# Kernel optimization log

Hardware: AMD Instinct MI355X
Metric: run time of the kernel (lower is better)

The kernel has to match this reference:

```python
import jax, jax.numpy as jnp
import numpy as np

B, C, H, Wd = 256, 2048, 14, 14
E, A = 16, 3000  # num experts (DESC_INDEX), num answers (ANSWER_INDEX)


def setup_inputs() -> dict:
    key = jax.random.key(0)
    k1, k2, k3, k4, k5 = jax.random.split(key, 5)
    return {
        "mask": jax.random.uniform(k1, (B, 1, H, Wd), dtype=jnp.float32),
        "features": jax.random.normal(k2, (B, C, H, Wd), dtype=jnp.float32),
        "W": jax.random.normal(k3, (E, A, C), dtype=jnp.float32) * 0.02,
        "b": jax.random.normal(k4, (E, A), dtype=jnp.float32) * 0.02,
        "inst": jax.random.randint(k5, (B,), 0, E, dtype=jnp.int64),
    }


def reference(mask, features, W, b, inst):
    Bn, Cn = features.shape[0], features.shape[1]
    feat = features.reshape(Bn, Cn, -1)          # [B, C, HW]
    m = mask.reshape(Bn, 1, -1) + 1e-10          # [B, 1, HW]
    # masked weighted average pool over spatial positions
    attended = (m * feat).sum(2) / m.sum(2)      # [B, C]
    # per-sample expert Linear: compute all experts via one GEMM, then gather
    logits = jnp.einsum('bc,eac->bea', attended, W) + b[None]  # [B, E, A]
    out = jnp.take_along_axis(logits, inst[:, None, None], axis=1)[:, 0, :]  # [B, A]
    return out
```

## Files before the change

kernel.cpp:

```cpp
#include <hip/hip_runtime.h>
#include <hip/hip_bf16.h>
#include <cstdint>

#define BN   256
#define CN   2048
#define HWN  196
#define EN   16
#define AN   3000

#define TS   32
#define TA   64
#define KC   32
#define LDST 36

__global__ __launch_bounds__(256) void pool_kernel(const float* __restrict__ mask,
                                                   const float* __restrict__ feat,
                                                   float* __restrict__ attended) {
    int wave = blockIdx.x * 4 + (threadIdx.x >> 6);
    int lane = threadIdx.x & 63;
    int b = wave / CN;
    int c = wave % CN;

    const float4* frow = (const float4*)(feat + ((size_t)b * CN + c) * HWN);
    const float4* mrow = (const float4*)(mask + (size_t)b * HWN);

    float num = 0.f, den = 0.f;
    if (lane < HWN / 4) {
        float4 f = frow[lane];
        float4 m = mrow[lane];
        float mx = m.x + 1e-10f, my = m.y + 1e-10f;
        float mz = m.z + 1e-10f, mw = m.w + 1e-10f;
        num = mx * f.x + my * f.y + mz * f.z + mw * f.w;
        den = mx + my + mz + mw;
    }
    #pragma unroll
    for (int off = 32; off; off >>= 1) {
        num += __shfl_xor(num, off, 64);
        den += __shfl_xor(den, off, 64);
    }
    if (lane == 0) attended[(size_t)b * CN + c] = num / den;
}

__global__ void group_kernel(const int* __restrict__ inst,
                             int* __restrict__ counts,
                             int* __restrict__ lists) {
    __shared__ int cnt[EN];
    int t = threadIdx.x;
    if (t < EN) cnt[t] = 0;
    __syncthreads();
    if (t < BN) {
        int e = inst[t];
        int pos = atomicAdd(&cnt[e], 1);
        lists[e * BN + pos] = t;
    }
    __syncthreads();
    if (t < EN) counts[t] = cnt[t];
}

__global__ __launch_bounds__(128) void gemm_kernel(const float* __restrict__ attended,
                                                   const float* __restrict__ W,
                                                   const float* __restrict__ bias,
                                                   const int* __restrict__ counts,
                                                   const int* __restrict__ lists,
                                                   float* __restrict__ out) {
    int e  = blockIdx.y;
    int a0 = blockIdx.x * TA;
    int n  = counts[e];
    if (n == 0) return;

    __shared__ float At[TS * LDST];
    __shared__ float Wt[TA * LDST];
    __shared__ int   sid[TS];

    int t  = threadIdx.x;
    int ts = t & 7;
    int ta = t >> 3;
    const int* lst = lists + e * BN;

    for (int s0 = 0; s0 < n; s0 += TS) {
        if (t < TS) sid[t] = (s0 + t < n) ? lst[s0 + t] : -1;

        float acc[4][4];
        #pragma unroll
        for (int i = 0; i < 4; i++)
            #pragma unroll
            for (int j = 0; j < 4; j++) acc[i][j] = 0.f;

        __syncthreads();

        for (int k0 = 0; k0 < CN; k0 += KC) {
            #pragma unroll
            for (int r = 0; r < 2; r++) {
                int q = t + r * 128;
                int row = q >> 3, pos = q & 7;
                int s = sid[row];
                float4 v = make_float4(0.f, 0.f, 0.f, 0.f);
                if (s >= 0) v = *(const float4*)(attended + (size_t)s * CN + k0 + pos * 4);
                *(float4*)(&At[row * LDST + pos * 4]) = v;
            }
            #pragma unroll
            for (int r = 0; r < 4; r++) {
                int q = t + r * 128;
                int row = q >> 3, pos = q & 7;
                int a = a0 + row;
                if (a < AN) {
                    float4 v = *(const float4*)(W + ((size_t)e * AN + a) * CN + k0 + pos * 4);
                    *(float4*)(&Wt[row * LDST + pos * 4]) = v;
                }
            }
            __syncthreads();

            #pragma unroll
            for (int kc = 0; kc < KC / 4; kc++) {
                float4 av[4], wv[4];
                #pragma unroll
                for (int i = 0; i < 4; i++)
                    av[i] = *(const float4*)(&At[(ts + 8 * i) * LDST + kc * 4]);
                #pragma unroll
                for (int j = 0; j < 4; j++)
                    wv[j] = *(const float4*)(&Wt[(ta + 16 * j) * LDST + kc * 4]);
                #pragma unroll
                for (int i = 0; i < 4; i++)
                    #pragma unroll
                    for (int j = 0; j < 4; j++) {
                        acc[i][j] += av[i].x * wv[j].x;
                        acc[i][j] += av[i].y * wv[j].y;
                        acc[i][j] += av[i].z * wv[j].z;
                        acc[i][j] += av[i].w * wv[j].w;
                    }
            }
            __syncthreads();
        }

        #pragma unroll
        for (int j = 0; j < 4; j++) {
            int a = a0 + ta + 16 * j;
            if (a < AN) {
                float bj = bias[e * AN + a];
                #pragma unroll
                for (int i = 0; i < 4; i++) {
                    int s = sid[ts + 8 * i];
                    if (s >= 0) out[(size_t)s * AN + a] = acc[i][j] + bj;
                }
            }
        }
        __syncthreads();
    }
}

extern "C" void kernel_launch(void* const* d_in, const int* in_sizes, int n_in,
                              void* d_out, int out_size, void* d_ws, size_t ws_size,
                              hipStream_t stream) {
    const float* mask = (const float*)d_in[0];
    const float* feat = (const float*)d_in[1];
    const float* W    = (const float*)d_in[2];
    const float* bias = (const float*)d_in[3];
    const int*   inst = (const int*)d_in[4];
    float* out = (float*)d_out;

    char* ws = (char*)d_ws;
    float* attended = (float*)ws;
    int*   counts   = (int*)(ws + (size_t)BN * CN * sizeof(float));
    int*   lists    = counts + EN;

    pool_kernel<<<BN * CN / 4, 256, 0, stream>>>(mask, feat, attended);

    group_kernel<<<1, 256, 0, stream>>>(inst, counts, lists);

    dim3 grid((AN + TA - 1) / TA, EN);
    gemm_kernel<<<grid, 128, 0, stream>>>(attended, W, bias, counts, lists, out);
}
```

Measured before the change: 957.6 us.

## Split-K expert GEMM with atomics, register prefetch, and multi-row pooling

The expert GEMM is split four ways along K across a new grid dimension. Partial sums are accumulated with atomicAdd into an output that a new kernel pre-fills with the per-sample bias. Global loads of the next K tile are prefetched into registers while the current tile is computed. The pooling kernel now handles eight channels per wave and uses a reciprocal denominator that a separate kernel computes once per batch row. This raises parallelism for the small-grid GEMM and overlaps loads with math, at the cost of atomic traffic, non-deterministic float summation order, and two extra launches.

```diff
diff --git a/kernel.cpp b/kernel.cpp
--- a/kernel.cpp
+++ b/kernel.cpp
@@ -1,5 +1,4 @@
 #include <hip/hip_runtime.h>
-#include <hip/hip_bf16.h>
 #include <cstdint>
 
 #define BN   256
@@ -12,33 +11,59 @@
 #define TA   64
 #define KC   32
 #define LDST 36
+#define KSPLIT 4
+#define KPART (CN / KSPLIT)
+
+#define RPW  8
+
+__global__ __launch_bounds__(256) void den_kernel(const float* __restrict__ mask,
+                                                  float* __restrict__ rden) {
+    int wave = blockIdx.x * 4 + (threadIdx.x >> 6);
+    int lane = threadIdx.x & 63;
+    float den = 0.f;
+    if (lane < HWN / 4) {
+        float4 m = ((const float4*)(mask + (size_t)wave * HWN))[lane];
+        den = (m.x + 1e-10f) + (m.y + 1e-10f) + (m.z + 1e-10f) + (m.w + 1e-10f);
+    }
+    #pragma unroll
+    for (int off = 32; off; off >>= 1) den += __shfl_xor(den, off, 64);
+    if (lane == 0) rden[wave] = 1.0f / den;
+}
 
 __global__ __launch_bounds__(256) void pool_kernel(const float* __restrict__ mask,
                                                    const float* __restrict__ feat,
+                                                   const float* __restrict__ rden,
                                                    float* __restrict__ attended) {
     int wave = blockIdx.x * 4 + (threadIdx.x >> 6);
     int lane = threadIdx.x & 63;
-    int b = wave / CN;
-    int c = wave % CN;
-
-    const float4* frow = (const float4*)(feat + ((size_t)b * CN + c) * HWN);
-    const float4* mrow = (const float4*)(mask + (size_t)b * HWN);
-
-    float num = 0.f, den = 0.f;
-    if (lane < HWN / 4) {
-        float4 f = frow[lane];
-        float4 m = mrow[lane];
-        float mx = m.x + 1e-10f, my = m.y + 1e-10f;
-        float mz = m.z + 1e-10f, mw = m.w + 1e-10f;
-        num = mx * f.x + my * f.y + mz * f.z + mw * f.w;
-        den = mx + my + mz + mw;
-    }
-    #pragma unroll
-    for (int off = 32; off; off >>= 1) {
-        num += __shfl_xor(num, off, 64);
-        den += __shfl_xor(den, off, 64);
-    }
-    if (lane == 0) attended[(size_t)b * CN + c] = num / den;
+    int b  = wave >> 8;
+    int c0 = (wave & 255) * RPW;
+    bool act = lane < HWN / 4;
+
+    float4 m = make_float4(0.f, 0.f, 0.f, 0.f);
+    if (act) {
+        m = ((const float4*)(mask + (size_t)b * HWN))[lane];
+        m.x += 1e-10f; m.y += 1e-10f; m.z += 1e-10f; m.w += 1e-10f;
+    }
+    const float4* fb = (const float4*)(feat + ((size_t)b * CN + c0) * HWN);
+    float4 f[RPW];
+    #pragma unroll
+    for (int r = 0; r < RPW; r++)
+        f[r] = act ? fb[r * (HWN / 4) + lane] : make_float4(0.f, 0.f, 0.f, 0.f);
+    float num[RPW];
+    #pragma unroll
+    for (int r = 0; r < RPW; r++)
+        num[r] = m.x * f[r].x + m.y * f[r].y + m.z * f[r].z + m.w * f[r].w;
+    #pragma unroll
+    for (int off = 32; off; off >>= 1)
+        #pragma unroll
+        for (int r = 0; r < RPW; r++) num[r] += __shfl_xor(num[r], off, 64);
+    if (lane == 0) {
+        float rd = rden[b];
+        #pragma unroll
+        for (int r = 0; r < RPW; r++)
+            attended[(size_t)b * CN + c0 + r] = num[r] * rd;
+    }
 }
 
 __global__ void group_kernel(const int* __restrict__ inst,
@@ -57,24 +82,38 @@
     if (t < EN) counts[t] = cnt[t];
 }
 
-__global__ __launch_bounds__(128) void gemm_kernel(const float* __restrict__ attended,
-                                                   const float* __restrict__ W,
-                                                   const float* __restrict__ bias,
-                                                   const int* __restrict__ counts,
-                                                   const int* __restrict__ lists,
-                                                   float* __restrict__ out) {
+__global__ __launch_bounds__(256) void bias_init_kernel(const float* __restrict__ bias,
+                                                        const int* __restrict__ inst,
+                                                        float* __restrict__ out) {
+    int b = blockIdx.x;
+    int e = inst[b];
+    const float4* br = (const float4*)(bias + (size_t)e * AN);
+    float4* orow = (float4*)(out + (size_t)b * AN);
+    for (int j = threadIdx.x; j < AN / 4; j += 256) orow[j] = br[j];
+}
+
+__global__ __launch_bounds__(128, 4) void gemm_kernel(const float* __restrict__ attended,
+                                                      const float* __restrict__ W,
+                                                      const int* __restrict__ counts,
+                                                      const int* __restrict__ lists,
+                                                      float* __restrict__ out) {
     int e  = blockIdx.y;
+    int kp = blockIdx.z;
     int a0 = blockIdx.x * TA;
     int n  = counts[e];
     if (n == 0) return;
+    int kbeg = kp * KPART;
+    int kend = kbeg + KPART;
 
     __shared__ float At[TS * LDST];
     __shared__ float Wt[TA * LDST];
     __shared__ int   sid[TS];
 
-    int t  = threadIdx.x;
-    int ts = t & 7;
-    int ta = t >> 3;
+    int t    = threadIdx.x;
+    int ts   = t & 7;
+    int ta   = t >> 3;
+    int srow = t >> 3;
+    int spos = t & 7;
     const int* lst = lists + e * BN;
 
     for (int s0 = 0; s0 < n; s0 += TS) {
@@ -88,27 +127,44 @@
 
         __syncthreads();
 
-        for (int k0 = 0; k0 < CN; k0 += KC) {
-            #pragma unroll
-            for (int r = 0; r < 2; r++) {
-                int q = t + r * 128;
-                int row = q >> 3, pos = q & 7;
-                int s = sid[row];
-                float4 v = make_float4(0.f, 0.f, 0.f, 0.f);
-                if (s >= 0) v = *(const float4*)(attended + (size_t)s * CN + k0 + pos * 4);
-                *(float4*)(&At[row * LDST + pos * 4]) = v;
-            }
-            #pragma unroll
-            for (int r = 0; r < 4; r++) {
-                int q = t + r * 128;
-                int row = q >> 3, pos = q & 7;
-                int a = a0 + row;
-                if (a < AN) {
-                    float4 v = *(const float4*)(W + ((size_t)e * AN + a) * CN + k0 + pos * 4);
-                    *(float4*)(&Wt[row * LDST + pos * 4]) = v;
+        float4 apre[2], wpre[4];
+        #pragma unroll
+        for (int r = 0; r < 2; r++) {
+            int s = sid[srow + 16 * r];
+            apre[r] = make_float4(0.f, 0.f, 0.f, 0.f);
+            if (s >= 0)
+                apre[r] = *(const float4*)(attended + (size_t)s * CN + kbeg + spos * 4);
+        }
+        #pragma unroll
+        for (int r = 0; r < 4; r++) {
+            int a = a0 + srow + 16 * r; if (a > AN - 1) a = AN - 1;
+            wpre[r] = *(const float4*)(W + ((size_t)e * AN + a) * CN + kbeg + spos * 4);
+        }
+
+        for (int k0 = kbeg; k0 < kend; k0 += KC) {
+            #pragma unroll
+            for (int r = 0; r < 2; r++)
+                *(float4*)(&At[(srow + 16 * r) * LDST + spos * 4]) = apre[r];
+            #pragma unroll
+            for (int r = 0; r < 4; r++)
+                *(float4*)(&Wt[(srow + 16 * r) * LDST + spos * 4]) = wpre[r];
+            __syncthreads();
+
+            if (k0 + KC < kend) {
+                int kn = k0 + KC;
+                #pragma unroll
+                for (int r = 0; r < 2; r++) {
+                    int s = sid[srow + 16 * r];
+                    apre[r] = make_float4(0.f, 0.f, 0.f, 0.f);
+                    if (s >= 0)
+                        apre[r] = *(const float4*)(attended + (size_t)s * CN + kn + spos * 4);
+                }
+                #pragma unroll
+                for (int r = 0; r < 4; r++) {
+                    int a = a0 + srow + 16 * r; if (a > AN - 1) a = AN - 1;
+                    wpre[r] = *(const float4*)(W + ((size_t)e * AN + a) * CN + kn + spos * 4);
                 }
             }
-            __syncthreads();
 
             #pragma unroll
             for (int kc = 0; kc < KC / 4; kc++) {
@@ -136,11 +192,10 @@
         for (int j = 0; j < 4; j++) {
             int a = a0 + ta + 16 * j;
             if (a < AN) {
-                float bj = bias[e * AN + a];
                 #pragma unroll
                 for (int i = 0; i < 4; i++) {
                     int s = sid[ts + 8 * i];
-                    if (s >= 0) out[(size_t)s * AN + a] = acc[i][j] + bj;
+                    if (s >= 0) atomicAdd(&out[(size_t)s * AN + a], acc[i][j]);
                 }
             }
         }
@@ -160,13 +215,14 @@
 
     char* ws = (char*)d_ws;
     float* attended = (float*)ws;
-    int*   counts   = (int*)(ws + (size_t)BN * CN * sizeof(float));
+    float* rden     = (float*)(ws + (size_t)BN * CN * sizeof(float));
+    int*   counts   = (int*)(rden + BN);
     int*   lists    = counts + EN;
 
-    pool_kernel<<<BN * CN / 4, 256, 0, stream>>>(mask, feat, attended);
-
+    den_kernel<<<BN / 4, 256, 0, stream>>>(mask, rden);
     group_kernel<<<1, 256, 0, stream>>>(inst, counts, lists);
-
-    dim3 grid((AN + TA - 1) / TA, EN);
-    gemm_kernel<<<grid, 128, 0, stream>>>(attended, W, bias, counts, lists, out);
-}
+    pool_kernel<<<BN * CN / RPW / 4, 256, 0, stream>>>(mask, feat, rden, attended);
+    bias_init_kernel<<<BN, 256, 0, stream>>>(bias, inst, out);
+    dim3 grid((AN + TA - 1) / TA, EN, KSPLIT);
+    gemm_kernel<<<grid, 128, 0, stream>>>(attended, W, counts, lists, out);
+}
```

Result: faster. 870.6 us (-9.1%).
